# Kernel tuning notes

Hardware: AMD Instinct MI355X
Metric: run time of the kernel (lower is better)

## Reference

```python
import jax, jax.numpy as jnp
import numpy as np

HIDDEN = 2048
N_HEADS = 16
HEAD_DIM = HIDDEN // N_HEADS
ROPE_BASE = 10000.0


def rotate_half(x):
    half = x.shape[-1] // 2
    return jnp.concatenate((-x[..., half:], x[..., :half]), axis=-1)


def rope_cos_sin(seq_len, dtype):
    inv_freq = 1.0 / (ROPE_BASE ** (jnp.arange(0, HEAD_DIM, 2, dtype=jnp.float32) / HEAD_DIM))
    pos = jnp.arange(seq_len, dtype=jnp.float32)
    freqs = jnp.einsum('i,j->ij', pos, inv_freq)  # [S, hd/2]
    emb = jnp.concatenate((freqs, freqs), axis=-1)  # [S, hd]
    return jnp.cos(emb).astype(dtype), jnp.sin(emb).astype(dtype)


def setup_inputs() -> dict:
    key = jax.random.key(0)
    ks = jax.random.split(key, 9)
    B, S, H = 2, 2048, HIDDEN
    std = 1.0 / np.sqrt(H)
    return {
        'hidden_states': jax.random.normal(ks[0], (B, S, H), dtype=jnp.float32),
        'Wq': jax.random.uniform(ks[1], (H, H), jnp.float32, -std, std),
        'bq': jax.random.uniform(ks[2], (H,), jnp.float32, -std, std),
        'Wk': jax.random.uniform(ks[3], (H, H), jnp.float32, -std, std),
        'bk': jax.random.uniform(ks[4], (H,), jnp.float32, -std, std),
        'Wv': jax.random.uniform(ks[5], (H, H), jnp.float32, -std, std),
        'bv': jax.random.uniform(ks[6], (H,), jnp.float32, -std, std),
        'Wo': jax.random.uniform(ks[7], (H, H), jnp.float32, -std, std),
        'bo': jax.random.uniform(ks[8], (H,), jnp.float32, -std, std),
    }


def reference(hidden_states, Wq, bq, Wk, bk, Wv, bv, Wo, bo):
    B, S, H = hidden_states.shape
    scale = HEAD_DIM ** -0.5

    def proj(W, b):
        # torch Linear: x @ W.T + b
        y = jnp.einsum('bsh,oh->bso', hidden_states, W) + b
        return y.reshape(B, S, N_HEADS, HEAD_DIM).transpose(0, 2, 1, 3)  # [B,nh,S,hd]

    q = proj(Wq, bq)
    k = proj(Wk, bk)
    v = proj(Wv, bv)

    cos, sin = rope_cos_sin(S, hidden_states.dtype)  # [S, hd]
    cos = cos[None, None, :, :]
    sin = sin[None, None, :, :]
    q = q * cos + rotate_half(q) * sin
    k = k * cos + rotate_half(k) * sin

    scores = jnp.einsum('bhqd,bhkd->bhqk', q, k) * scale  # [B,nh,S,S]
    probs = jax.nn.softmax(scores, axis=-1)
    ctx = jnp.einsum('bhqk,bhkd->bhqd', probs, v)
    ctx = ctx.transpose(0, 2, 1, 3).reshape(B, S, H)
    return jnp.einsum('bsh,oh->bso', ctx, Wo) + bo
```

## Files before the change

kernel.cpp:

```cpp
#include <hip/hip_runtime.h>
#include <hip/hip_bf16.h>
#include <math.h>

#define HIDDEN 2048
#define NH 16
#define HD 128
#define NB 2
#define SEQ 2048
#define K_DIM 2048

typedef unsigned int u32;
typedef unsigned short ushort_t;
typedef __bf16 bf16x8 __attribute__((ext_vector_type(8)));
typedef float f32x4 __attribute__((ext_vector_type(4)));
typedef ushort_t u16x8 __attribute__((ext_vector_type(8)));

__device__ __forceinline__ void split1(float x, unsigned short& h, unsigned short& l) {
    u32 u = __float_as_uint(x);
    u32 hr = (u + 0x7FFFu + ((u >> 16) & 1u)) >> 16;
    h = (unsigned short)hr;
    float r = x - __uint_as_float(hr << 16);
    u32 u2 = __float_as_uint(r);
    l = (unsigned short)((u2 + 0x7FFFu + ((u2 >> 16) & 1u)) >> 16);
}

__device__ __forceinline__ ushort_t bf16r(float x) {
    u32 u = __float_as_uint(x);
    return (ushort_t)((u + 0x7FFFu + ((u >> 16) & 1u)) >> 16);
}

__device__ __forceinline__ float bf2f(ushort_t u) {
    return __uint_as_float(((u32)u) << 16);
}

__device__ __forceinline__ void gl_lds16(const void* g, void* l) {
    __builtin_amdgcn_global_load_lds(
        (const __attribute__((address_space(1))) u32*)g,
        (__attribute__((address_space(3))) u32*)l, 16, 0, 0);
}

__global__ void k_rope_tables(float* __restrict__ ct, float* __restrict__ st) {
    int idx = blockIdx.x * 256 + threadIdx.x;
    int s = idx >> 6, d = idx & 63;
    double inv = pow(10000.0, -(double)d * (1.0 / 64.0));
    double ang = (double)s * inv;
    ct[idx] = (float)cos(ang);
    st[idx] = (float)sin(ang);
}

#define XG 2097152
#define WG 1048576
__global__ void k_cvt_all(const float4* __restrict__ X, const float4* __restrict__ W0,
                          const float4* __restrict__ W1, const float4* __restrict__ W2,
                          const float4* __restrict__ Wo,
                          ushort4* __restrict__ Xh, ushort4* __restrict__ H0,
                          ushort4* __restrict__ H1, ushort4* __restrict__ H2,
                          ushort4* __restrict__ WoH, ushort4* __restrict__ WoL) {
    int idx = blockIdx.x * 256 + threadIdx.x;
    if (idx < XG + 3 * WG) {
        const float4* src;
        ushort4* dst;
        int off;
        if (idx < XG) { src = X; dst = Xh; off = idx; }
        else {
            int t = idx - XG;
            int m = t >> 20;
            off = t & (WG - 1);
            src = (m == 0) ? W0 : (m == 1) ? W1 : W2;
            dst = (m == 0) ? H0 : (m == 1) ? H1 : H2;
        }
        float4 x = src[off];
        ushort4 h;
        h.x = bf16r(x.x); h.y = bf16r(x.y); h.z = bf16r(x.z); h.w = bf16r(x.w);
        dst[off] = h;
    } else {
        int off = idx - XG - 3 * WG;
        float4 x = Wo[off];
        ushort4 h, l;
        split1(x.x, h.x, l.x);
        split1(x.y, h.y, l.y);
        split1(x.z, h.z, l.z);
        split1(x.w, h.w, l.w);
        WoH[off] = h;
        WoL[off] = l;
    }
}

#define BAR  __builtin_amdgcn_s_barrier()
#define VM6  asm volatile("s_waitcnt vmcnt(6)" ::: "memory")
#define VM4  asm volatile("s_waitcnt vmcnt(4)" ::: "memory")
#define VM0  asm volatile("s_waitcnt vmcnt(0)" ::: "memory")
#define PRIO1 __builtin_amdgcn_s_setprio(1)
#define PRIO0 __builtin_amdgcn_s_setprio(0)

#define QSTAGE(slot, kt) do { \
    const ushort_t* gA_ = Xh + sgA + (size_t)(kt) * 32; \
    gl_lds16(gA_, &As[slot][(w * 32) * 32]); \
    gl_lds16(gA_ + 16 * 2048, &As[slot][(w * 32 + 16) * 32]); \
    const ushort_t* gB_ = Wsel + sgB + (size_t)(kt) * 32; \
    gl_lds16(gB_, &Bs[slot][(w * 32) * 32]); \
    gl_lds16(gB_ + 16 * 2048, &Bs[slot][(w * 32 + 16) * 32]); \
} while (0)

#define QRD(AD, BD, slot) do { \
    _Pragma("unroll") for (int mf = 0; mf < 8; mf++) \
        AD[mf] = *(const bf16x8*)&As[slot][arow + mf * 512 + ccq]; \
    _Pragma("unroll") for (int nf = 0; nf < 4; nf++) \
        BD[nf] = *(const bf16x8*)&Bs[slot][brow + nf * 512 + ccq]; \
} while (0)

#define QMFMA(AD, BD) do { PRIO1; \
    _Pragma("unroll") for (int mf = 0; mf < 8; mf++) \
    _Pragma("unroll") for (int nf = 0; nf < 4; nf++) \
        acc[mf][nf] = __builtin_amdgcn_mfma_f32_16x16x32_bf16( \
            AD[mf], BD[nf], acc[mf][nf], 0, 0, 0); \
    PRIO0; } while (0)

__global__ __launch_bounds__(512, 2)
void k_gemm_qkv8(const ushort_t* __restrict__ Xh,
                 const ushort_t* __restrict__ W0, const ushort_t* __restrict__ W1,
                 const ushort_t* __restrict__ W2,
                 const float* __restrict__ b0, const float* __restrict__ b1,
                 const float* __restrict__ b2,
                 ushort_t* __restrict__ o0, ushort_t* __restrict__ o1,
                 ushort_t* __restrict__ o2) {
    __shared__ ushort_t As[4][256 * 32];
    __shared__ ushort_t Bs[4][256 * 32];
    const int tid = threadIdx.x;
    const int lane = tid & 63;
    const int w = tid >> 6;
    const int wm = w >> 2;
    const int wn = w & 3;
    const int quad = lane >> 4;
    const int l15 = lane & 15;

    int bid = blockIdx.x;
    bid = (bid & 7) * 48 + (bid >> 3);
    const int bx = bid & 15;
    const int by = bid >> 4;
    const int m0 = bx << 8;
    const int mat = by >> 3;
    const int n0 = (by & 7) << 8;
    const ushort_t* Wsel = (mat == 0) ? W0 : (mat == 1) ? W1 : W2;
    const float* bias = (mat == 0) ? b0 : (mat == 1) ? b1 : b2;
    ushort_t* out = (mat == 0) ? o0 : (mat == 1) ? o1 : o2;

    const int lrow4 = lane >> 2;
    const int col8 = (((lane & 3) ^ ((lrow4 >> 1) & 3)) << 3);
    const size_t sgA = (size_t)(m0 + w * 32 + lrow4) * 2048 + col8;
    const size_t sgB = (size_t)(n0 + w * 32 + lrow4) * 2048 + col8;

    const int arow = (wm * 128 + l15) * 32;
    const int brow = (wn * 64 + l15) * 32;
    const int ccq = ((quad ^ ((l15 >> 1) & 3)) << 3);

    f32x4 acc[8][4];
#pragma unroll
    for (int i = 0; i < 8; i++)
#pragma unroll
        for (int j = 0; j < 4; j++) acc[i][j] = (f32x4){0.f, 0.f, 0.f, 0.f};

    bf16x8 aA[8], bA[4], aB[8], bB[4];

    QSTAGE(0, 0); QSTAGE(1, 1);
    VM4; BAR;
    QRD(aA, bA, 0);

    for (int p = 0; p < 60; p += 4) {
        QSTAGE(2, p + 2); VM4; BAR; QRD(aB, bB, 1); QMFMA(aA, bA);
        QSTAGE(3, p + 3); VM4; BAR; QRD(aA, bA, 2); QMFMA(aB, bB);
        QSTAGE(0, p + 4); VM4; BAR; QRD(aB, bB, 3); QMFMA(aA, bA);
        QSTAGE(1, p + 5); VM4; BAR; QRD(aA, bA, 0); QMFMA(aB, bB);
    }
    QSTAGE(2, 62); VM4; BAR; QRD(aB, bB, 1); QMFMA(aA, bA);
    QSTAGE(3, 63); VM4; BAR; QRD(aA, bA, 2); QMFMA(aB, bB);
    VM0; BAR;                QRD(aB, bB, 3); QMFMA(aA, bA);
    QMFMA(aB, bB);

    float bcolv[4];
#pragma unroll
    for (int nf = 0; nf < 4; nf++) bcolv[nf] = bias[n0 + wn * 64 + nf * 16 + l15];

    const int mbase = m0 + wm * 128 + quad * 4;
#pragma unroll
    for (int mf = 0; mf < 8; mf++)
#pragma unroll
        for (int nf = 0; nf < 4; nf++) {
            const int n = n0 + wn * 64 + nf * 16 + l15;
            const int hh = n >> 7;
            const int d = n & 127;
#pragma unroll
            for (int r = 0; r < 4; r++) {
                const int m = mbase + mf * 16 + r;
                const int bb = m >> 11;
                const int s = m & (SEQ - 1);
                out[((size_t)(bb * NH + hh) * SEQ + s) * HD + d] =
                    bf16r(acc[mf][nf][r] + bcolv[nf]);
            }
        }
}

#define OSTAGE(slot, kt) do { \
    const size_t koA = (size_t)((kt) >> 2) * ((size_t)SEQ * HD) + (size_t)((kt) & 3) * 32; \
    const size_t koB = (size_t)(kt) * 32; \
    gl_lds16(Ah + sgA0 + koA, &Ah_s[slot][(w * 32) * 32]); \
    gl_lds16(Ah + sgA0 + 16 * HD + koA, &Ah_s[slot][(w * 32 + 16) * 32]); \
    gl_lds16(Al + sgA0 + koA, &Al_s[slot][(w * 32) * 32]); \
    gl_lds16(Al + sgA0 + 16 * HD + koA, &Al_s[slot][(w * 32 + 16) * 32]); \
    gl_lds16(Bh + sgB0 + koB, &Bh_s[slot][(w * 16) * 32]); \
    gl_lds16(Bl + sgB0 + koB, &Bl_s[slot][(w * 16) * 32]); \
} while (0)

#define ORD(AH, AL, BH, BL, slot) do { \
    _Pragma("unroll") for (int f = 0; f < 4; f++) { \
        AH[f] = *(const bf16x8*)&Ah_s[slot][aro + f * 512 + cco]; \
        AL[f] = *(const bf16x8*)&Al_s[slot][aro + f * 512 + cco]; \
        BH[f] = *(const bf16x8*)&Bh_s[slot][bro + f * 512 + cco]; \
        BL[f] = *(const bf16x8*)&Bl_s[slot][bro + f * 512 + cco]; \
    } \
} while (0)

#define OMFMA(AH, AL, BH, BL) do { PRIO1; \
    _Pragma("unroll") for (int mf = 0; mf < 4; mf++) \
    _Pragma("unroll") for (int nf = 0; nf < 4; nf++) { \
        acc[mf][nf] = __builtin_amdgcn_mfma_f32_16x16x32_bf16( \
            AH[mf], BH[nf], acc[mf][nf], 0, 0, 0); \
        acc[mf][nf] = __builtin_amdgcn_mfma_f32_16x16x32_bf16( \
            AH[mf], BL[nf], acc[mf][nf], 0, 0, 0); \
        acc[mf][nf] = __builtin_amdgcn_mfma_f32_16x16x32_bf16( \
            AL[mf], BH[nf], acc[mf][nf], 0, 0, 0); \
    } PRIO0; } while (0)

__global__ __launch_bounds__(512, 2)
void k_gemm_o2(const ushort_t* __restrict__ Ah, const ushort_t* __restrict__ Al,
               const ushort_t* __restrict__ Bh, const ushort_t* __restrict__ Bl,
               const float* __restrict__ bias, float* __restrict__ out) {
    __shared__ ushort_t Ah_s[3][256 * 32];
    __shared__ ushort_t Al_s[3][256 * 32];
    __shared__ ushort_t Bh_s[3][128 * 32];
    __shared__ ushort_t Bl_s[3][128 * 32];
    const int tid = threadIdx.x;
    const int lane = tid & 63;
    const int w = tid >> 6;
    const int wm = w >> 1;
    const int wn = w & 1;
    const int quad = lane >> 4;
    const int l15 = lane & 15;

    int bid = blockIdx.x;
    bid = (bid & 7) * 32 + (bid >> 3);
    const int bx = bid & 15;
    const int by = bid >> 4;
    const int m0 = bx << 8;
    const int n0 = by << 7;

    const int lrow4 = lane >> 2;
    const int col8 = (((lane & 3) ^ ((lrow4 >> 1) & 3)) << 3);
    const size_t sgA0 = ((size_t)(m0 >> 11) * NH * SEQ + (size_t)((m0 & (SEQ - 1)) + w * 32 + lrow4)) * HD + col8;
    const size_t sgB0 = (size_t)(n0 + w * 16 + lrow4) * K_DIM + col8;

    const int aro = (wm * 64 + l15) * 32;
    const int bro = (wn * 64 + l15) * 32;
    const int cco = ((quad ^ ((l15 >> 1) & 3)) << 3);

    f32x4 acc[4][4];
#pragma unroll
    for (int i = 0; i < 4; i++)
#pragma unroll
        for (int j = 0; j < 4; j++) acc[i][j] = (f32x4){0.f, 0.f, 0.f, 0.f};

    bf16x8 ahA[4], alA[4], bhA[4], blA[4];
    bf16x8 ahB[4], alB[4], bhB[4], blB[4];

    OSTAGE(0, 0);
    OSTAGE(1, 1);
    VM6; BAR;
    ORD(ahA, alA, bhA, blA, 0);

    for (int it = 0; it < 10; ++it) {
        const int q = 6 * it;
        VM0; BAR; OSTAGE(2, q + 2); ORD(ahB, alB, bhB, blB, 1); OMFMA(ahA, alA, bhA, blA);
        VM0; BAR; OSTAGE(0, q + 3); ORD(ahA, alA, bhA, blA, 2); OMFMA(ahB, alB, bhB, blB);
        VM0; BAR; OSTAGE(1, q + 4); ORD(ahB, alB, bhB, blB, 0); OMFMA(ahA, alA, bhA, blA);
        VM0; BAR; OSTAGE(2, q + 5); ORD(ahA, alA, bhA, blA, 1); OMFMA(ahB, alB, bhB, blB);
        VM0; BAR; OSTAGE(0, q + 6); ORD(ahB, alB, bhB, blB, 2); OMFMA(ahA, alA, bhA, blA);
        VM0; BAR; OSTAGE(1, q + 7); ORD(ahA, alA, bhA, blA, 0); OMFMA(ahB, alB, bhB, blB);
    }
    VM0; BAR; OSTAGE(2, 62); ORD(ahB, alB, bhB, blB, 1); OMFMA(ahA, alA, bhA, blA);
    VM0; BAR; OSTAGE(0, 63); ORD(ahA, alA, bhA, blA, 2); OMFMA(ahB, alB, bhB, blB);
    VM0; BAR;                ORD(ahB, alB, bhB, blB, 0); OMFMA(ahA, alA, bhA, blA);
    OMFMA(ahB, alB, bhB, blB);

    float bcolv[4];
#pragma unroll
    for (int nf = 0; nf < 4; nf++) bcolv[nf] = bias[n0 + wn * 64 + nf * 16 + l15];

    const int mb = m0 + wm * 64 + quad * 4;
    const int nb = n0 + wn * 64 + l15;
#pragma unroll
    for (int fm = 0; fm < 4; fm++)
#pragma unroll
        for (int fn = 0; fn < 4; fn++)
#pragma unroll
            for (int r = 0; r < 4; r++)
                out[(size_t)(mb + fm * 16 + r) * HIDDEN + nb + fn * 16] =
                    acc[fm][fn][r] + bcolv[fn];
}

__global__ __launch_bounds__(256)
void k_rope_vpack(const ushort_t* __restrict__ qb, const ushort_t* __restrict__ kb,
                  const ushort_t* __restrict__ vb,
                  const float* __restrict__ ct, const float* __restrict__ st,
                  ushort_t* __restrict__ Qb, ushort_t* __restrict__ Kb,
                  ushort_t* __restrict__ vt) {
    __shared__ float t[64][65];
    const int tid = threadIdx.x;
    const int blk = blockIdx.x;
    if (blk < 16384) {
        int idx = blk * 256 + tid;
        int d = idx & 63;
        int s = (idx >> 6) & (SEQ - 1);
        int bh = idx >> 17;
        size_t base = ((size_t)bh * SEQ + s) * HD;
        float c = ct[(s << 6) + d], sn = st[(s << 6) + d];
        const float scq = 0.08838834764831845f;
        float q0 = bf2f(qb[base + d]), q1 = bf2f(qb[base + d + 64]);
        Qb[base + d]      = bf16r((q0 * c - q1 * sn) * scq);
        Qb[base + d + 64] = bf16r((q1 * c + q0 * sn) * scq);
        float k0 = bf2f(kb[base + d]), k1 = bf2f(kb[base + d + 64]);
        Kb[base + d]      = bf16r(k0 * c - k1 * sn);
        Kb[base + d + 64] = bf16r(k1 * c + k0 * sn);
    } else {
        int b = blk - 16384;
        const int s0 = (b & 31) << 6;
        const int d0 = ((b >> 5) & 1) << 6;
        const int bh = b >> 6;
        const ushort_t* src = vb + ((size_t)bh * SEQ + s0) * HD + d0;
        const int rr = tid >> 4;
        const int cc = (tid & 15) << 2;
#pragma unroll
        for (int i = 0; i < 4; i++) {
            ushort4 x = *(const ushort4*)(src + (size_t)(i * 16 + rr) * HD + cc);
            t[i * 16 + rr][cc]     = bf2f(x.x);
            t[i * 16 + rr][cc + 1] = bf2f(x.y);
            t[i * 16 + rr][cc + 2] = bf2f(x.z);
            t[i * 16 + rr][cc + 3] = bf2f(x.w);
        }
        __syncthreads();
        const int dr = tid >> 2;
        const int sc_ = (tid & 3) << 4;
        ushort_t* dst = vt + ((size_t)bh * HD + d0 + dr) * SEQ + s0 + sc_;
        u16x8 o0, o1;
#pragma unroll
        for (int u = 0; u < 8; u++) o0[u] = bf16r(t[sc_ + u][dr]);
#pragma unroll
        for (int u = 0; u < 8; u++) o1[u] = bf16r(t[sc_ + 8 + u][dr]);
        *(u16x8*)dst = o0;
        *(u16x8*)(dst + 8) = o1;
    }
}

__global__ __launch_bounds__(256, 2)
void k_flash_mfma(const ushort_t* __restrict__ Qb, const ushort_t* __restrict__ Kb,
                  const ushort_t* __restrict__ Vt,
                  ushort_t* __restrict__ ch, ushort_t* __restrict__ cl) {
    __shared__ ushort_t SH[27136];
    ushort_t* Ks = SH;
    ushort_t* Vs = SH + 8704;
    ushort_t* Ps = SH + 17920;
    const int tid = threadIdx.x;
    const int lane = tid & 63;
    const int w = tid >> 6;
    const int quad = lane >> 4;
    const int l15 = lane & 15;
    const int bi = blockIdx.x;
    const int bh = bi & 31;
    const int qt = bi >> 5;
    const ushort_t* Qg = Qb + ((size_t)bh * SEQ + ((size_t)qt << 7)) * HD;
    const ushort_t* Kg = Kb + (size_t)bh * SEQ * HD;
    const ushort_t* Vg = Vt + (size_t)bh * HD * SEQ;

    bf16x8 qf[2][4];
#pragma unroll
    for (int qi = 0; qi < 2; qi++)
#pragma unroll
        for (int ks = 0; ks < 4; ks++)
            qf[qi][ks] = *(const bf16x8*)(Qg + (size_t)(w * 32 + qi * 16 + l15) * HD + ks * 32 + quad * 8);

    const int sr = tid >> 4;
    const int sc8 = (tid & 15) << 3;
    const int vr = tid >> 3;
    const int vc8 = (tid & 7) << 3;

    u16x8 Kreg[4], Vreg[4];
#pragma unroll
    for (int i = 0; i < 4; i++)
        Kreg[i] = *(const u16x8*)(Kg + (size_t)(i * 16 + sr) * HD + sc8);
#pragma unroll
    for (int i = 0; i < 4; i++)
        Vreg[i] = *(const u16x8*)(Vg + (size_t)(i * 32 + vr) * SEQ + vc8);

    f32x4 acc[2][8];
#pragma unroll
    for (int qi = 0; qi < 2; qi++)
#pragma unroll
        for (int d = 0; d < 8; d++) acc[qi][d] = (f32x4){0.f, 0.f, 0.f, 0.f};
    float lp[2] = {0.f, 0.f};

    for (int kt = 0; kt < SEQ; kt += 64) {
        const int np = kt + 64;
        __syncthreads();
#pragma unroll
        for (int i = 0; i < 4; i++)
            *(u16x8*)&Ks[(i * 16 + sr) * 136 + sc8] = Kreg[i];
#pragma unroll
        for (int i = 0; i < 4; i++)
            *(u16x8*)&Vs[(i * 32 + vr) * 72 + vc8] = Vreg[i];
        if (np < SEQ) {
#pragma unroll
            for (int i = 0; i < 4; i++)
                Kreg[i] = *(const u16x8*)(Kg + (size_t)(np + i * 16 + sr) * HD + sc8);
#pragma unroll
            for (int i = 0; i < 4; i++)
                Vreg[i] = *(const u16x8*)(Vg + (size_t)(i * 32 + vr) * SEQ + np + vc8);
        }
        __syncthreads();

        f32x4 sc[2][4];
#pragma unroll
        for (int qi = 0; qi < 2; qi++)
#pragma unroll
            for (int j = 0; j < 4; j++) sc[qi][j] = (f32x4){0.f, 0.f, 0.f, 0.f};
#pragma unroll
        for (int ks = 0; ks < 4; ks++) {
            bf16x8 kf[4];
#pragma unroll
            for (int j = 0; j < 4; j++)
                kf[j] = *(const bf16x8*)&Ks[(j * 16 + l15) * 136 + ks * 32 + quad * 8];
#pragma unroll
            for (int qi = 0; qi < 2; qi++)
#pragma unroll
                for (int j = 0; j < 4; j++)
                    sc[qi][j] = __builtin_amdgcn_mfma_f32_16x16x32_bf16(
                        kf[j], qf[qi][ks], sc[qi][j], 0, 0, 0);
        }

#pragma unroll
        for (int qi = 0; qi < 2; qi++) {
            const int prow = (w * 32 + qi * 16 + l15) * 72 + quad * 4;
#pragma unroll
            for (int j = 0; j < 4; j++) {
                float p0 = __expf(sc[qi][j][0]);
                float p1 = __expf(sc[qi][j][1]);
                float p2 = __expf(sc[qi][j][2]);
                float p3 = __expf(sc[qi][j][3]);
                lp[qi] += (p0 + p1) + (p2 + p3);
                __hip_bfloat162 lo2 = __float22bfloat162_rn({p0, p1});
                __hip_bfloat162 hi2 = __float22bfloat162_rn({p2, p3});
                uint2 pk = make_uint2(*(u32*)&lo2, *(u32*)&hi2);
                *(uint2*)&Ps[prow + j * 16] = pk;
            }
        }

#pragma unroll
        for (int ks = 0; ks < 2; ks++) {
            bf16x8 pf[2];
#pragma unroll
            for (int qi = 0; qi < 2; qi++)
                pf[qi] = *(const bf16x8*)&Ps[(w * 32 + qi * 16 + l15) * 72 + ks * 32 + quad * 8];
#pragma unroll
            for (int db = 0; db < 8; db++) {
                bf16x8 vf = *(const bf16x8*)&Vs[(db * 16 + l15) * 72 + ks * 32 + quad * 8];
#pragma unroll
                for (int qi = 0; qi < 2; qi++)
                    acc[qi][db] = __builtin_amdgcn_mfma_f32_16x16x32_bf16(vf, pf[qi], acc[qi][db], 0, 0, 0);
            }
        }
    }

    float inv[2];
#pragma unroll
    for (int qi = 0; qi < 2; qi++) {
        float l = lp[qi];
        l += __shfl_xor(l, 16);
        l += __shfl_xor(l, 32);
        inv[qi] = 1.0f / l;
    }
    const size_t obase = ((size_t)bh * SEQ + ((size_t)qt << 7)) * HD;

    __syncthreads();
#pragma unroll
    for (int qi = 0; qi < 2; qi++)
#pragma unroll
        for (int db = 0; db < 8; db++) {
            ushort4 hh;
            ushort_t dum;
            split1(acc[qi][db][0] * inv[qi], hh.x, dum);
            split1(acc[qi][db][1] * inv[qi], hh.y, dum);
            split1(acc[qi][db][2] * inv[qi], hh.z, dum);
            split1(acc[qi][db][3] * inv[qi], hh.w, dum);
            *(ushort4*)&SH[(w * 32 + qi * 16 + l15) * 136 + db * 16 + quad * 4] = hh;
        }
    __syncthreads();
#pragma unroll
    for (int t2 = 0; t2 < 8; t2++) {
        int c = t2 * 256 + tid;
        int row = c >> 4, col8 = (c & 15) << 3;
        *(u16x8*)&ch[obase + (size_t)row * HD + col8] = *(const u16x8*)&SH[row * 136 + col8];
    }
    __syncthreads();
#pragma unroll
    for (int qi = 0; qi < 2; qi++)
#pragma unroll
        for (int db = 0; db < 8; db++) {
            ushort4 ll;
            ushort_t dum;
            split1(acc[qi][db][0] * inv[qi], dum, ll.x);
            split1(acc[qi][db][1] * inv[qi], dum, ll.y);
            split1(acc[qi][db][2] * inv[qi], dum, ll.z);
            split1(acc[qi][db][3] * inv[qi], dum, ll.w);
            *(ushort4*)&SH[(w * 32 + qi * 16 + l15) * 136 + db * 16 + quad * 4] = ll;
        }
    __syncthreads();
#pragma unroll
    for (int t2 = 0; t2 < 8; t2++) {
        int c = t2 * 256 + tid;
        int row = c >> 4, col8 = (c & 15) << 3;
        *(u16x8*)&cl[obase + (size_t)row * HD + col8] = *(const u16x8*)&SH[row * 136 + col8];
    }
}

extern "C" void kernel_launch(void* const* d_in, const int* in_sizes, int n_in,
                              void* d_out, int out_size, void* d_ws, size_t ws_size,
                              hipStream_t stream) {
    const float* X  = (const float*)d_in[0];
    const float* Wq = (const float*)d_in[1];
    const float* bq = (const float*)d_in[2];
    const float* Wk = (const float*)d_in[3];
    const float* bk = (const float*)d_in[4];
    const float* Wv = (const float*)d_in[5];
    const float* bv = (const float*)d_in[6];
    const float* Wo = (const float*)d_in[7];
    const float* bo = (const float*)d_in[8];
    float* out = (float*)d_out;

    const size_t QS = (size_t)NB * NH * SEQ * HD;
    const size_t WS = (size_t)HIDDEN * HIDDEN;
    ushort_t* qb_ws = (ushort_t*)d_ws;
    ushort_t* kb_ws = qb_ws + QS;
    ushort_t* vb_ws = kb_ws + QS;
    float* cost = (float*)(vb_ws + QS);
    float* sint = cost + (size_t)SEQ * 64;
    ushort_t* Xh = (ushort_t*)(sint + (size_t)SEQ * 64);
    ushort_t* Wh0 = Xh + QS;
    ushort_t* Wh1 = Wh0 + WS;
    ushort_t* Wh2 = Wh1 + WS;
    ushort_t* Woh = Wh2 + WS;
    ushort_t* Wol = Woh + WS;
    ushort_t* Kb  = Wol + WS;
    ushort_t* Vtb = Kb + QS;
    ushort_t* ctxh = qb_ws;
    ushort_t* ctxl = kb_ws;

    k_rope_tables<<<(SEQ * 64) / 256, 256, 0, stream>>>(cost, sint);

    k_cvt_all<<<(XG + 4 * WG) / 256, 256, 0, stream>>>(
        (const float4*)X, (const float4*)Wq, (const float4*)Wk, (const float4*)Wv,
        (const float4*)Wo,
        (ushort4*)Xh, (ushort4*)Wh0, (ushort4*)Wh1, (ushort4*)Wh2,
        (ushort4*)Woh, (ushort4*)Wol);

    k_gemm_qkv8<<<384, 512, 0, stream>>>(Xh, Wh0, Wh1, Wh2, bq, bk, bv,
                                         qb_ws, kb_ws, vb_ws);

    ushort_t* Qbb = Xh;
    k_rope_vpack<<<16384 + 2048, 256, 0, stream>>>(qb_ws, kb_ws, vb_ws, cost, sint,
                                                   Qbb, Kb, Vtb);

    k_flash_mfma<<<512, 256, 0, stream>>>(Qbb, Kb, Vtb, ctxh, ctxl);

    k_gemm_o2<<<dim3(256), 512, 0, stream>>>(ctxh, ctxl, Woh, Wol, bo, out);
}
```

Measured before the change: 469.7 us.

## Fuse Q RoPE into flash kernel, vectorize K RoPE, merge table kernel

The flash-attention kernel now loads raw Q, applies RoPE and the softmax scale in registers, and packs the result straight into its MFMA fragments. This removes a separate Q RoPE pass that read and wrote a full Q buffer. K RoPE is rewritten so each thread handles 8 elements with vector loads, which shrinks that part of the grid from 16384 to 2048 blocks. RoPE table generation moves into the conversion kernel as extra blocks, saving one launch. The ctx output buffer is redirected to Xh so it does not overwrite the raw Q that the flash kernel still needs to read.

New measurement: 446.7 us. -4.9%, faster.

```diff
diff --git a/kernel.cpp b/kernel.cpp
--- a/kernel.cpp
+++ b/kernel.cpp
@@ -39,24 +39,27 @@
         (__attribute__((address_space(3))) u32*)l, 16, 0, 0);
 }
 
-__global__ void k_rope_tables(float* __restrict__ ct, float* __restrict__ st) {
-    int idx = blockIdx.x * 256 + threadIdx.x;
-    int s = idx >> 6, d = idx & 63;
-    double inv = pow(10000.0, -(double)d * (1.0 / 64.0));
-    double ang = (double)s * inv;
-    ct[idx] = (float)cos(ang);
-    st[idx] = (float)sin(ang);
-}
-
 #define XG 2097152
 #define WG 1048576
+#define TBLK 512
 __global__ void k_cvt_all(const float4* __restrict__ X, const float4* __restrict__ W0,
                           const float4* __restrict__ W1, const float4* __restrict__ W2,
                           const float4* __restrict__ Wo,
                           ushort4* __restrict__ Xh, ushort4* __restrict__ H0,
                           ushort4* __restrict__ H1, ushort4* __restrict__ H2,
-                          ushort4* __restrict__ WoH, ushort4* __restrict__ WoL) {
-    int idx = blockIdx.x * 256 + threadIdx.x;
+                          ushort4* __restrict__ WoH, ushort4* __restrict__ WoL,
+                          float* __restrict__ ct, float* __restrict__ st) {
+    const int blk = blockIdx.x;
+    if (blk < TBLK) {
+        int idx = blk * 256 + threadIdx.x;
+        int s = idx >> 6, d = idx & 63;
+        double inv = pow(10000.0, -(double)d * (1.0 / 64.0));
+        double ang = (double)s * inv;
+        ct[idx] = (float)cos(ang);
+        st[idx] = (float)sin(ang);
+        return;
+    }
+    int idx = (blk - TBLK) * 256 + threadIdx.x;
     if (idx < XG + 3 * WG) {
         const float4* src;
         ushort4* dst;
@@ -308,30 +311,37 @@
 }
 
 __global__ __launch_bounds__(256)
-void k_rope_vpack(const ushort_t* __restrict__ qb, const ushort_t* __restrict__ kb,
-                  const ushort_t* __restrict__ vb,
-                  const float* __restrict__ ct, const float* __restrict__ st,
-                  ushort_t* __restrict__ Qb, ushort_t* __restrict__ Kb,
-                  ushort_t* __restrict__ vt) {
+void k_ropek_vpack(const ushort_t* __restrict__ kb, const ushort_t* __restrict__ vb,
+                   const float* __restrict__ ct, const float* __restrict__ st,
+                   ushort_t* __restrict__ Kb, ushort_t* __restrict__ vt) {
     __shared__ float t[64][65];
     const int tid = threadIdx.x;
     const int blk = blockIdx.x;
-    if (blk < 16384) {
+    if (blk < 2048) {
         int idx = blk * 256 + tid;
-        int d = idx & 63;
-        int s = (idx >> 6) & (SEQ - 1);
-        int bh = idx >> 17;
+        int o = idx & 7;
+        int s = (idx >> 3) & (SEQ - 1);
+        int bh = idx >> 14;
+        const int d0 = o << 3;
         size_t base = ((size_t)bh * SEQ + s) * HD;
-        float c = ct[(s << 6) + d], sn = st[(s << 6) + d];
-        const float scq = 0.08838834764831845f;
-        float q0 = bf2f(qb[base + d]), q1 = bf2f(qb[base + d + 64]);
-        Qb[base + d]      = bf16r((q0 * c - q1 * sn) * scq);
-        Qb[base + d + 64] = bf16r((q1 * c + q0 * sn) * scq);
-        float k0 = bf2f(kb[base + d]), k1 = bf2f(kb[base + d + 64]);
-        Kb[base + d]      = bf16r(k0 * c - k1 * sn);
-        Kb[base + d + 64] = bf16r(k1 * c + k0 * sn);
+        float c[8], sn[8];
+        *(float4*)&c[0]  = *(const float4*)&ct[(s << 6) + d0];
+        *(float4*)&c[4]  = *(const float4*)&ct[(s << 6) + d0 + 4];
+        *(float4*)&sn[0] = *(const float4*)&st[(s << 6) + d0];
+        *(float4*)&sn[4] = *(const float4*)&st[(s << 6) + d0 + 4];
+        u16x8 k0 = *(const u16x8*)(kb + base + d0);
+        u16x8 k1 = *(const u16x8*)(kb + base + 64 + d0);
+        u16x8 lo, hi;
+#pragma unroll
+        for (int j = 0; j < 8; j++) {
+            float a = bf2f(k0[j]), b = bf2f(k1[j]);
+            lo[j] = bf16r(a * c[j] - b * sn[j]);
+            hi[j] = bf16r(b * c[j] + a * sn[j]);
+        }
+        *(u16x8*)(Kb + base + d0) = lo;
+        *(u16x8*)(Kb + base + 64 + d0) = hi;
     } else {
-        int b = blk - 16384;
+        int b = blk - 2048;
         const int s0 = (b & 31) << 6;
         const int d0 = ((b >> 5) & 1) << 6;
         const int bh = b >> 6;
@@ -363,6 +373,7 @@
 __global__ __launch_bounds__(256, 2)
 void k_flash_mfma(const ushort_t* __restrict__ Qb, const ushort_t* __restrict__ Kb,
                   const ushort_t* __restrict__ Vt,
+                  const float* __restrict__ ct, const float* __restrict__ st,
                   ushort_t* __restrict__ ch, ushort_t* __restrict__ cl) {
     __shared__ ushort_t SH[27136];
     ushort_t* Ks = SH;
@@ -380,12 +391,42 @@
     const ushort_t* Kg = Kb + (size_t)bh * SEQ * HD;
     const ushort_t* Vg = Vt + (size_t)bh * HD * SEQ;
 
+    const float scq = 0.08838834764831845f;
     bf16x8 qf[2][4];
 #pragma unroll
-    for (int qi = 0; qi < 2; qi++)
-#pragma unroll
-        for (int ks = 0; ks < 4; ks++)
-            qf[qi][ks] = *(const bf16x8*)(Qg + (size_t)(w * 32 + qi * 16 + l15) * HD + ks * 32 + quad * 8);
+    for (int qi = 0; qi < 2; qi++) {
+        const int row = w * 32 + qi * 16 + l15;
+        const int sg = (qt << 7) + row;
+        const int tb = (sg << 6) + quad * 8;
+        float c0[8], s0[8], c1[8], s1[8];
+        *(float4*)&c0[0] = *(const float4*)&ct[tb];
+        *(float4*)&c0[4] = *(const float4*)&ct[tb + 4];
+        *(float4*)&s0[0] = *(const float4*)&st[tb];
+        *(float4*)&s0[4] = *(const float4*)&st[tb + 4];
+        *(float4*)&c1[0] = *(const float4*)&ct[tb + 32];
+        *(float4*)&c1[4] = *(const float4*)&ct[tb + 36];
+        *(float4*)&s1[0] = *(const float4*)&st[tb + 32];
+        *(float4*)&s1[4] = *(const float4*)&st[tb + 36];
+        const ushort_t* qrow = Qg + (size_t)row * HD + quad * 8;
+        u16x8 r0 = *(const u16x8*)(qrow);
+        u16x8 r1 = *(const u16x8*)(qrow + 32);
+        u16x8 r2 = *(const u16x8*)(qrow + 64);
+        u16x8 r3 = *(const u16x8*)(qrow + 96);
+        u16x8 f0, f1, f2, f3;
+#pragma unroll
+        for (int j = 0; j < 8; j++) {
+            float a0 = bf2f(r0[j]), a1 = bf2f(r1[j]);
+            float a2 = bf2f(r2[j]), a3 = bf2f(r3[j]);
+            f0[j] = bf16r((a0 * c0[j] - a2 * s0[j]) * scq);
+            f2[j] = bf16r((a2 * c0[j] + a0 * s0[j]) * scq);
+            f1[j] = bf16r((a1 * c1[j] - a3 * s1[j]) * scq);
+            f3[j] = bf16r((a3 * c1[j] + a1 * s1[j]) * scq);
+        }
+        qf[qi][0] = __builtin_bit_cast(bf16x8, f0);
+        qf[qi][1] = __builtin_bit_cast(bf16x8, f1);
+        qf[qi][2] = __builtin_bit_cast(bf16x8, f2);
+        qf[qi][3] = __builtin_bit_cast(bf16x8, f3);
+    }
 
     const int sr = tid >> 4;
     const int sc8 = (tid & 15) << 3;
@@ -559,25 +600,21 @@
     ushort_t* Wol = Woh + WS;
     ushort_t* Kb  = Wol + WS;
     ushort_t* Vtb = Kb + QS;
-    ushort_t* ctxh = qb_ws;
+    ushort_t* ctxh = Xh;
     ushort_t* ctxl = kb_ws;
 
-    k_rope_tables<<<(SEQ * 64) / 256, 256, 0, stream>>>(cost, sint);
-
-    k_cvt_all<<<(XG + 4 * WG) / 256, 256, 0, stream>>>(
+    k_cvt_all<<<TBLK + (XG + 4 * WG) / 256, 256, 0, stream>>>(
         (const float4*)X, (const float4*)Wq, (const float4*)Wk, (const float4*)Wv,
         (const float4*)Wo,
         (ushort4*)Xh, (ushort4*)Wh0, (ushort4*)Wh1, (ushort4*)Wh2,
-        (ushort4*)Woh, (ushort4*)Wol);
+        (ushort4*)Woh, (ushort4*)Wol, cost, sint);
 
     k_gemm_qkv8<<<384, 512, 0, stream>>>(Xh, Wh0, Wh1, Wh2, bq, bk, bv,
                                          qb_ws, kb_ws, vb_ws);
 
-    ushort_t* Qbb = Xh;
-    k_rope_vpack<<<16384 + 2048, 256, 0, stream>>>(qb_ws, kb_ws, vb_ws, cost, sint,
-                                                   Qbb, Kb, Vtb);
-
-    k_flash_mfma<<<512, 256, 0, stream>>>(Qbb, Kb, Vtb, ctxh, ctxl);
+    k_ropek_vpack<<<4096, 256, 0, stream>>>(kb_ws, vb_ws, cost, sint, Kb, Vtb);
+
+    k_flash_mfma<<<512, 256, 0, stream>>>(qb_ws, Kb, Vtb, cost, sint, ctxh, ctxl);
 
     k_gemm_o2<<<dim3(256), 512, 0, stream>>>(ctxh, ctxl, Woh, Wol, bo, out);
 }
```
